# Kernel tuning notes

Hardware: AMD Instinct MI355X
Metric: run time of the kernel (lower is better)

Reference implementation:

```python
import jax, jax.numpy as jnp
import numpy as np

DIM_BODY = 10
DIM_OBJECT = 15
NB_OBJECTS = 3
FIRST_INDS = np.array([0,1,2,3,4,5,6,7,8,9,10,11,12,13,15,16,17,20,21,25])
SECOND_INDS = np.array([0,1,2,3,4,5,6,7,8,9,14,18,19,22,23,24,26,27,28,29])
LOG_SIG_MIN, LOG_SIG_MAX = -20.0, 2.0


def setup_inputs() -> dict:
    key = jax.random.key(0)
    ks = jax.random.split(key, 16)
    B = 65536
    s = 0.05  # weight scale, keeps activations sane
    return {
        "obs": jax.random.normal(ks[0], (B, DIM_BODY + NB_OBJECTS * DIM_OBJECT), jnp.float32),
        "ag": jax.random.normal(ks[1], (B, 30), jnp.float32),
        "g": jax.random.normal(ks[2], (B, 30), jnp.float32),
        "phi_w1": jax.random.normal(ks[3], (80, 256), jnp.float32) * s,
        "phi_b1": jnp.zeros((256,), jnp.float32),
        "phi_w2": jax.random.normal(ks[4], (256, 256), jnp.float32) * s,
        "phi_b2": jnp.zeros((256,), jnp.float32),
        "rho_w1": jax.random.normal(ks[5], (256, 256), jnp.float32) * s,
        "rho_b1": jnp.zeros((256,), jnp.float32),
        "mean_w": jax.random.normal(ks[6], (256, 4), jnp.float32) * s,
        "mean_b": jnp.zeros((4,), jnp.float32),
        "logstd_w": jax.random.normal(ks[7], (256, 4), jnp.float32) * s,
        "logstd_b": jnp.zeros((4,), jnp.float32),
    }


def reference(obs, ag, g, phi_w1, phi_b1, phi_w2, phi_b2, rho_w1, rho_b1,
              mean_w, mean_b, logstd_w, logstd_b):
    body = obs[:, :DIM_BODY]  # [B,10]
    objs = [obs[:, DIM_BODY + DIM_OBJECT * i: DIM_BODY + DIM_OBJECT * (i + 1)]
            for i in range(NB_OBJECTS)]
    ag_f, g_f = ag[:, FIRST_INDS], g[:, FIRST_INDS]
    ag_s, g_s = ag[:, SECOND_INDS], g[:, SECOND_INDS]
    pair_inputs = []
    for i in range(NB_OBJECTS):
        for j in range(NB_OBJECTS):
            if i < j:
                pair_inputs.append(jnp.concatenate([ag_f, body, g_f, objs[i], objs[j]], axis=1))
            elif j < i:
                pair_inputs.append(jnp.concatenate([ag_s, body, g_s, objs[i], objs[j]], axis=1))
    inp = jnp.stack(pair_inputs)  # [6, B, 80]
    # shared phi MLP (2 layers, ReLU on both)
    h = jax.nn.relu(jnp.einsum('pbi,ih->pbh', inp, phi_w1) + phi_b1)
    phi = jax.nn.relu(jnp.einsum('pbh,ho->pbo', h, phi_w2) + phi_b2)
    agg = phi.sum(axis=0)  # [B, 256] sum over pairs
    # rho head
    hr = jax.nn.relu(agg @ rho_w1 + rho_b1)
    mean = hr @ mean_w + mean_b
    logstd = jnp.clip(hr @ logstd_w + logstd_b, LOG_SIG_MIN, LOG_SIG_MAX)
    return mean, logstd
```

## Files before the change

kernel.cpp:

```cpp
#include <hip/hip_runtime.h>
#include <hip/hip_bf16.h>


#define B_TOTAL 65536
#define TROWS   64
#define RSTR    136

typedef __attribute__((ext_vector_type(8))) short s8v;
typedef __attribute__((ext_vector_type(4))) float f4v;

__constant__ int c_PI[6] = {0,0,1,1,2,2};
__constant__ int c_PJ[6] = {1,2,0,2,0,1};
__constant__ int c_PF[6] = {0,0,1,0,1,1};
__constant__ int c_INV[2][30] = {
  {0,1,2,3,4,5,6,7,8,9,10,11,12,13,-1,14,15,16,-1,-1,17,18,-1,-1,-1,19,-1,-1,-1,-1},
  {0,1,2,3,4,5,6,7,8,9,-1,-1,-1,-1,10,-1,-1,-1,11,12,-1,-1,13,14,15,-1,16,17,18,19}};

__global__ void prep_weights(const float* __restrict__ phi_w1,
                             const float* __restrict__ phi_b1,
                             const float* __restrict__ phi_w2,
                             const float* __restrict__ rho_w1,
                             const float* __restrict__ mean_w,
                             const float* __restrict__ logstd_w,
                             __hip_bfloat16* __restrict__ W1P,
                             __hip_bfloat16* __restrict__ W2f,
                             __hip_bfloat16* __restrict__ W3f,
                             __hip_bfloat16* __restrict__ W4f) {
  const int i0 = blockIdx.x * blockDim.x + threadIdx.x;
  const int stride = gridDim.x * blockDim.x;
  for (int d = i0; d < 6 * 32768; d += stride) {
    int p = d >> 15, r = d & 32767;
    int j = r & 7, lane = (r >> 3) & 63, blk = r >> 9;
    int nb = blk >> 2, ks = blk & 3;
    int n = nb * 16 + (lane & 15), k = ks * 32 + (lane >> 4) * 8 + j;
    int f = c_PF[p], oi = c_PI[p], oj = c_PJ[p];
    float v = 0.0f;
    if (k < 30)       { int t = c_INV[f][k];      if (t >= 0) v = phi_w1[t * 256 + n]; }
    else if (k < 60)  { int t = c_INV[f][k - 30]; if (t >= 0) v = phi_w1[(30 + t) * 256 + n]; }
    else if (k < 70)  { v = phi_w1[(20 + k - 60) * 256 + n]; }
    else if (k < 115) { int q = (k - 70) / 15, t = (k - 70) - q * 15;
                        int c = (q == oi) ? 50 + t : (q == oj) ? 65 + t : -1;
                        if (c >= 0) v = phi_w1[c * 256 + n]; }
    else if (k == 115) v = phi_b1[n];
    W1P[d] = __float2bfloat16(v);
  }
  for (int d = i0; d < 65536; d += stride) {
    int j = d & 7, lane = (d >> 3) & 63, blk = d >> 9;
    int nb = blk >> 3, ks = blk & 7;
    int n = nb * 16 + (lane & 15), k = ks * 32 + (lane >> 4) * 8 + j;
    W2f[d] = __float2bfloat16(phi_w2[k * 256 + n]);
    W3f[d] = __float2bfloat16(rho_w1[k * 256 + n]);
  }
  for (int d = i0; d < 4096; d += stride) {
    int j = d & 7, lane = (d >> 3) & 63, ks = d >> 9;
    int n = lane & 15, k = ks * 32 + (lane >> 4) * 8 + j;
    float v = (n < 4) ? mean_w[k * 4 + n]
            : (n < 8) ? logstd_w[k * 4 + (n - 4)] : 0.0f;
    W4f[d] = __float2bfloat16(v);
  }
}

static __device__ __forceinline__ unsigned pk2(float a, float b) {
  __hip_bfloat162 h = __float22bfloat162_rn(float2{a, b});
  union { __hip_bfloat162 h2; unsigned u; } cv; cv.h2 = h;
  return cv.u;
}

__global__ __launch_bounds__(512, 2)
void actor_main(const float* __restrict__ obs, const float* __restrict__ ag,
                const float* __restrict__ g,
                const __hip_bfloat16* __restrict__ W1P,
                const __hip_bfloat16* __restrict__ W2f,
                const __hip_bfloat16* __restrict__ W3f,
                const __hip_bfloat16* __restrict__ W4f,
                const float* __restrict__ b2, const float* __restrict__ b3,
                const float* __restrict__ meanb,
                const float* __restrict__ logstdb,
                float* __restrict__ out) {
  __shared__ __align__(16) __hip_bfloat16 HsBuf[2][4 * 8 * 512];

  const int tid  = threadIdx.x;
  const int lane = tid & 63;
  const int w    = tid >> 6;
  const int l15  = lane & 15;
  const int quad = lane >> 4;
  const int r0   = blockIdx.x * TROWS;

  float4 b2v[2];
#pragma unroll
  for (int i = 0; i < 2; ++i)
    b2v[i] = *(const float4*)&b2[w * 32 + i * 16 + quad * 4];

  s8v w2f[8][2];
#pragma unroll
  for (int i = 0; i < 2; ++i)
#pragma unroll
    for (int ks = 0; ks < 8; ++ks)
      w2f[ks][i] = *(const s8v*)&W2f[(((w * 2 + i) * 8 + ks) * 512) + lane * 8];

  {
    __hip_bfloat16* rawS = &HsBuf[0][0];
    const int row = tid >> 3;
    const int c0  = (tid & 7) * 16;
    const float* agr = ag  + (size_t)(r0 + row) * 30;
    const float* gr  = g   + (size_t)(r0 + row) * 30;
    const float* obr = obs + (size_t)(r0 + row) * 55;
#pragma unroll
    for (int cc = 0; cc < 16; ++cc) {
      int c = c0 + cc;
      float v;
      if      (c < 30)  v = agr[c];
      else if (c < 60)  v = gr[c - 30];
      else if (c < 115) v = obr[c - 60];
      else if (c == 115) v = 1.0f;
      else              v = 0.0f;
      rawS[row * RSTR + c] = __float2bfloat16(v);
    }
  }
  __syncthreads();

  s8v bxr[4][4];
  {
    const __hip_bfloat16* rawS = &HsBuf[0][0];
#pragma unroll
    for (int ks = 0; ks < 4; ++ks)
#pragma unroll
      for (int rt = 0; rt < 4; ++rt)
        bxr[ks][rt] = *(const s8v*)&rawS[(rt * 16 + l15) * RSTR + ks * 32 + quad * 8];
  }
  __syncthreads();

  f4v agg[2][4];
#pragma unroll
  for (int i = 0; i < 2; ++i)
#pragma unroll
    for (int rt = 0; rt < 4; ++rt) agg[i][rt] = f4v{0.f, 0.f, 0.f, 0.f};

  const int ebase = l15 * 8 + (quad >> 1) * 128 + (quad & 1) * 4;

#pragma unroll 1
  for (int p = 0; p < 6; ++p) {
    __hip_bfloat16* buf = &HsBuf[p & 1][0];
    const __hip_bfloat16* w1base = W1P + p * 32768;

#pragma unroll
    for (int i = 0; i < 2; ++i) {
      s8v w1f[4];
#pragma unroll
      for (int ks = 0; ks < 4; ++ks)
        w1f[ks] = *(const s8v*)&w1base[(((w * 2 + i) * 4 + ks) * 512) + lane * 8];
      f4v h[4];
#pragma unroll
      for (int rt = 0; rt < 4; ++rt) h[rt] = f4v{0.f, 0.f, 0.f, 0.f};
#pragma unroll
      for (int ks = 0; ks < 4; ++ks)
#pragma unroll
        for (int rt = 0; rt < 4; ++rt)
          h[rt] = __builtin_amdgcn_mfma_f32_16x16x32_bf16(w1f[ks], bxr[ks][rt], h[rt], 0, 0, 0);
#pragma unroll
      for (int rt = 0; rt < 4; ++rt) {
        float v0 = fmaxf(h[rt][0], 0.f);
        float v1 = fmaxf(h[rt][1], 0.f);
        float v2 = fmaxf(h[rt][2], 0.f);
        float v3 = fmaxf(h[rt][3], 0.f);
        uint2 U; U.x = pk2(v0, v1); U.y = pk2(v2, v3);
        *reinterpret_cast<uint2*>(&buf[(rt * 8 + w) * 512 + i * 256 + ebase]) = U;
      }
    }
    __syncthreads();

    f4v a2[2][4];
#pragma unroll
    for (int i = 0; i < 2; ++i)
#pragma unroll
      for (int rt = 0; rt < 4; ++rt) a2[i][rt] = f4v{0.f, 0.f, 0.f, 0.f};
#pragma unroll
    for (int ks = 0; ks < 8; ++ks) {
      s8v hf[4];
#pragma unroll
      for (int rt = 0; rt < 4; ++rt)
        hf[rt] = *(const s8v*)&buf[(rt * 8 + ks) * 512 + lane * 8];
#pragma unroll
      for (int i = 0; i < 2; ++i)
#pragma unroll
        for (int rt = 0; rt < 4; ++rt)
          a2[i][rt] = __builtin_amdgcn_mfma_f32_16x16x32_bf16(w2f[ks][i], hf[rt], a2[i][rt], 0, 0, 0);
    }
#pragma unroll
    for (int i = 0; i < 2; ++i)
#pragma unroll
      for (int rt = 0; rt < 4; ++rt) {
        agg[i][rt][0] += fmaxf(a2[i][rt][0] + b2v[i].x, 0.f);
        agg[i][rt][1] += fmaxf(a2[i][rt][1] + b2v[i].y, 0.f);
        agg[i][rt][2] += fmaxf(a2[i][rt][2] + b2v[i].z, 0.f);
        agg[i][rt][3] += fmaxf(a2[i][rt][3] + b2v[i].w, 0.f);
      }
  }

  s8v w3f[8][2];
#pragma unroll
  for (int i = 0; i < 2; ++i)
#pragma unroll
    for (int ks = 0; ks < 8; ++ks)
      w3f[ks][i] = *(const s8v*)&W3f[(((w * 2 + i) * 8 + ks) * 512) + lane * 8];
  float4 b3v[2];
#pragma unroll
  for (int i = 0; i < 2; ++i)
    b3v[i] = *(const float4*)&b3[w * 32 + i * 16 + quad * 4];

  {
    __hip_bfloat16* bufA = &HsBuf[0][0];
#pragma unroll
    for (int i = 0; i < 2; ++i)
#pragma unroll
      for (int rt = 0; rt < 4; ++rt) {
        uint2 U; U.x = pk2(agg[i][rt][0], agg[i][rt][1]);
        U.y = pk2(agg[i][rt][2], agg[i][rt][3]);
        *reinterpret_cast<uint2*>(&bufA[(rt * 8 + w) * 512 + i * 256 + ebase]) = U;
      }
  }
  __syncthreads();

  f4v a3[2][4];
#pragma unroll
  for (int i = 0; i < 2; ++i)
#pragma unroll
    for (int rt = 0; rt < 4; ++rt) a3[i][rt] = f4v{0.f, 0.f, 0.f, 0.f};
  {
    const __hip_bfloat16* bufA = &HsBuf[0][0];
#pragma unroll
    for (int ks = 0; ks < 8; ++ks) {
      s8v hf[4];
#pragma unroll
      for (int rt = 0; rt < 4; ++rt)
        hf[rt] = *(const s8v*)&bufA[(rt * 8 + ks) * 512 + lane * 8];
#pragma unroll
      for (int i = 0; i < 2; ++i)
#pragma unroll
        for (int rt = 0; rt < 4; ++rt)
          a3[i][rt] = __builtin_amdgcn_mfma_f32_16x16x32_bf16(w3f[ks][i], hf[rt], a3[i][rt], 0, 0, 0);
    }
  }
  {
    __hip_bfloat16* bufB = &HsBuf[1][0];
#pragma unroll
    for (int i = 0; i < 2; ++i)
#pragma unroll
      for (int rt = 0; rt < 4; ++rt) {
        float v0 = fmaxf(a3[i][rt][0] + b3v[i].x, 0.f);
        float v1 = fmaxf(a3[i][rt][1] + b3v[i].y, 0.f);
        float v2 = fmaxf(a3[i][rt][2] + b3v[i].z, 0.f);
        float v3 = fmaxf(a3[i][rt][3] + b3v[i].w, 0.f);
        uint2 U; U.x = pk2(v0, v1); U.y = pk2(v2, v3);
        *reinterpret_cast<uint2*>(&bufB[(rt * 8 + w) * 512 + i * 256 + ebase]) = U;
      }
  }
  __syncthreads();

  if (w < 4) {
    const __hip_bfloat16* bufB = &HsBuf[1][0];
    f4v a4 = f4v{0.f, 0.f, 0.f, 0.f};
#pragma unroll
    for (int ks = 0; ks < 8; ++ks) {
      s8v w4 = *(const s8v*)&W4f[ks * 512 + lane * 8];
      s8v hf = *(const s8v*)&bufB[(w * 8 + ks) * 512 + lane * 8];
      a4 = __builtin_amdgcn_mfma_f32_16x16x32_bf16(w4, hf, a4, 0, 0, 0);
    }
    const int row = r0 + w * 16 + l15;
    if (quad == 0) {
      float4 mb = *(const float4*)meanb;
      float4 o;
      o.x = a4[0] + mb.x; o.y = a4[1] + mb.y;
      o.z = a4[2] + mb.z; o.w = a4[3] + mb.w;
      *reinterpret_cast<float4*>(&out[(size_t)row * 4]) = o;
    } else if (quad == 1) {
      float4 lb = *(const float4*)logstdb;
      float4 o;
      o.x = fminf(fmaxf(a4[0] + lb.x, -20.f), 2.f);
      o.y = fminf(fmaxf(a4[1] + lb.y, -20.f), 2.f);
      o.z = fminf(fmaxf(a4[2] + lb.z, -20.f), 2.f);
      o.w = fminf(fmaxf(a4[3] + lb.w, -20.f), 2.f);
      *reinterpret_cast<float4*>(&out[(size_t)B_TOTAL * 4 + (size_t)row * 4]) = o;
    }
  }
}

extern "C" void kernel_launch(void* const* d_in, const int* in_sizes, int n_in,
                              void* d_out, int out_size, void* d_ws, size_t ws_size,
                              hipStream_t stream) {
  const float* obs      = (const float*)d_in[0];
  const float* ag       = (const float*)d_in[1];
  const float* g        = (const float*)d_in[2];
  const float* phi_w1   = (const float*)d_in[3];
  const float* phi_b1   = (const float*)d_in[4];
  const float* phi_w2   = (const float*)d_in[5];
  const float* phi_b2   = (const float*)d_in[6];
  const float* rho_w1   = (const float*)d_in[7];
  const float* rho_b1   = (const float*)d_in[8];
  const float* mean_w   = (const float*)d_in[9];
  const float* mean_b   = (const float*)d_in[10];
  const float* logstd_w = (const float*)d_in[11];
  const float* logstd_b = (const float*)d_in[12];
  float* out = (float*)d_out;

  char* ws = (char*)d_ws;
  __hip_bfloat16* W1P = (__hip_bfloat16*)(ws);
  __hip_bfloat16* W2f = (__hip_bfloat16*)(ws + 393216);
  __hip_bfloat16* W3f = (__hip_bfloat16*)(ws + 393216 + 131072);
  __hip_bfloat16* W4f = (__hip_bfloat16*)(ws + 393216 + 262144);

  prep_weights<<<256, 256, 0, stream>>>(phi_w1, phi_b1, phi_w2, rho_w1,
                                        mean_w, logstd_w, W1P, W2f, W3f, W4f);
  actor_main<<<B_TOTAL / TROWS, 512, 0, stream>>>(
      obs, ag, g, W1P, W2f, W3f, W4f, phi_b2, rho_b1, mean_b, logstd_b, out);
}
```

Before: 195.8 us.

## Prefetch next pair's W1 fragments, keep raw inputs in LDS, vectorize prep

Each pair iteration now loads the next pair's layer-1 weight fragments into registers while the current pair computes, hiding global-load latency. Raw inputs move to a dedicated LDS buffer and are re-read per pair instead of being held as 16 register fragments. The input staging and prep_weights kernel now write 16-byte vectors, with prep using one output fragment per wave. The changes trade extra LDS space and reads, plus the double-buffered weight registers, for fewer stalls; register pressure at 512 threads x 2 blocks may spill or cut occupancy.

```diff
diff --git a/kernel.cpp b/kernel.cpp
--- a/kernel.cpp
+++ b/kernel.cpp
@@ -16,48 +16,77 @@
   {0,1,2,3,4,5,6,7,8,9,10,11,12,13,-1,14,15,16,-1,-1,17,18,-1,-1,-1,19,-1,-1,-1,-1},
   {0,1,2,3,4,5,6,7,8,9,-1,-1,-1,-1,10,-1,-1,-1,11,12,-1,-1,13,14,15,-1,16,17,18,19}};
 
-__global__ void prep_weights(const float* __restrict__ phi_w1,
-                             const float* __restrict__ phi_b1,
-                             const float* __restrict__ phi_w2,
-                             const float* __restrict__ rho_w1,
-                             const float* __restrict__ mean_w,
-                             const float* __restrict__ logstd_w,
-                             __hip_bfloat16* __restrict__ W1P,
-                             __hip_bfloat16* __restrict__ W2f,
-                             __hip_bfloat16* __restrict__ W3f,
-                             __hip_bfloat16* __restrict__ W4f) {
-  const int i0 = blockIdx.x * blockDim.x + threadIdx.x;
-  const int stride = gridDim.x * blockDim.x;
-  for (int d = i0; d < 6 * 32768; d += stride) {
-    int p = d >> 15, r = d & 32767;
-    int j = r & 7, lane = (r >> 3) & 63, blk = r >> 9;
-    int nb = blk >> 2, ks = blk & 3;
-    int n = nb * 16 + (lane & 15), k = ks * 32 + (lane >> 4) * 8 + j;
-    int f = c_PF[p], oi = c_PI[p], oj = c_PJ[p];
-    float v = 0.0f;
-    if (k < 30)       { int t = c_INV[f][k];      if (t >= 0) v = phi_w1[t * 256 + n]; }
-    else if (k < 60)  { int t = c_INV[f][k - 30]; if (t >= 0) v = phi_w1[(30 + t) * 256 + n]; }
-    else if (k < 70)  { v = phi_w1[(20 + k - 60) * 256 + n]; }
-    else if (k < 115) { int q = (k - 70) / 15, t = (k - 70) - q * 15;
-                        int c = (q == oi) ? 50 + t : (q == oj) ? 65 + t : -1;
-                        if (c >= 0) v = phi_w1[c * 256 + n]; }
-    else if (k == 115) v = phi_b1[n];
-    W1P[d] = __float2bfloat16(v);
-  }
-  for (int d = i0; d < 65536; d += stride) {
-    int j = d & 7, lane = (d >> 3) & 63, blk = d >> 9;
-    int nb = blk >> 3, ks = blk & 7;
-    int n = nb * 16 + (lane & 15), k = ks * 32 + (lane >> 4) * 8 + j;
-    W2f[d] = __float2bfloat16(phi_w2[k * 256 + n]);
-    W3f[d] = __float2bfloat16(rho_w1[k * 256 + n]);
-  }
-  for (int d = i0; d < 4096; d += stride) {
-    int j = d & 7, lane = (d >> 3) & 63, ks = d >> 9;
-    int n = lane & 15, k = ks * 32 + (lane >> 4) * 8 + j;
-    float v = (n < 4) ? mean_w[k * 4 + n]
-            : (n < 8) ? logstd_w[k * 4 + (n - 4)] : 0.0f;
-    W4f[d] = __float2bfloat16(v);
-  }
+static __device__ __forceinline__ short bf16s(float v) {
+  __hip_bfloat16 h = __float2bfloat16(v);
+  union { __hip_bfloat16 h; short s; } u; u.h = h; return u.s;
+}
+
+__global__ __launch_bounds__(256)
+void prep_weights(const float* __restrict__ phi_w1,
+                  const float* __restrict__ phi_b1,
+                  const float* __restrict__ phi_w2,
+                  const float* __restrict__ rho_w1,
+                  const float* __restrict__ mean_w,
+                  const float* __restrict__ logstd_w,
+                  __hip_bfloat16* __restrict__ W1P,
+                  __hip_bfloat16* __restrict__ W2f,
+                  __hip_bfloat16* __restrict__ W3f,
+                  __hip_bfloat16* __restrict__ W4f) {
+  const int wid  = (blockIdx.x * blockDim.x + threadIdx.x) >> 6;
+  const int lane = threadIdx.x & 63;
+  const int l15  = lane & 15;
+  const int kq   = (lane >> 4) * 8;
+  if (wid >= 648) return;
+  union { short s[8]; s8v v; } o;
+  __hip_bfloat16* dst;
+  if (wid < 384) {
+    const int p = wid >> 6, rem = wid & 63;
+    const int nb = rem >> 2, ks = rem & 3;
+    const int n = nb * 16 + l15;
+    const int f = c_PF[p], oi = c_PI[p], oj = c_PJ[p];
+#pragma unroll
+    for (int j = 0; j < 8; ++j) {
+      int k = ks * 32 + kq + j;
+      float v = 0.0f;
+      if (k < 30)       { int t = c_INV[f][k];      if (t >= 0) v = phi_w1[t * 256 + n]; }
+      else if (k < 60)  { int t = c_INV[f][k - 30]; if (t >= 0) v = phi_w1[(30 + t) * 256 + n]; }
+      else if (k < 70)  { v = phi_w1[(20 + k - 60) * 256 + n]; }
+      else if (k < 115) { int q = (k - 70) / 15, t = (k - 70) - q * 15;
+                          int c = (q == oi) ? 50 + t : (q == oj) ? 65 + t : -1;
+                          if (c >= 0) v = phi_w1[c * 256 + n]; }
+      else if (k == 115) v = phi_b1[n];
+      o.s[j] = bf16s(v);
+    }
+    dst = W1P + wid * 512 + lane * 8;
+  } else if (wid < 512) {
+    const int r = wid - 384;
+    const int nb = r >> 3, ks = r & 7;
+    const int n = nb * 16 + l15;
+#pragma unroll
+    for (int j = 0; j < 8; ++j)
+      o.s[j] = bf16s(phi_w2[(ks * 32 + kq + j) * 256 + n]);
+    dst = W2f + r * 512 + lane * 8;
+  } else if (wid < 640) {
+    const int r = wid - 512;
+    const int nb = r >> 3, ks = r & 7;
+    const int n = nb * 16 + l15;
+#pragma unroll
+    for (int j = 0; j < 8; ++j)
+      o.s[j] = bf16s(rho_w1[(ks * 32 + kq + j) * 256 + n]);
+    dst = W3f + r * 512 + lane * 8;
+  } else {
+    const int ks = wid - 640;
+    const int n = l15;
+#pragma unroll
+    for (int j = 0; j < 8; ++j) {
+      int k = ks * 32 + kq + j;
+      float v = (n < 4) ? mean_w[k * 4 + n]
+              : (n < 8) ? logstd_w[k * 4 + (n - 4)] : 0.0f;
+      o.s[j] = bf16s(v);
+    }
+    dst = W4f + ks * 512 + lane * 8;
+  }
+  *reinterpret_cast<s8v*>(dst) = o.v;
 }
 
 static __device__ __forceinline__ unsigned pk2(float a, float b) {
@@ -77,6 +106,7 @@
                 const float* __restrict__ meanb,
                 const float* __restrict__ logstdb,
                 float* __restrict__ out) {
+  __shared__ __align__(16) __hip_bfloat16 rawS[TROWS * RSTR];
   __shared__ __align__(16) __hip_bfloat16 HsBuf[2][4 * 8 * 512];
 
   const int tid  = threadIdx.x;
@@ -99,12 +129,12 @@
       w2f[ks][i] = *(const s8v*)&W2f[(((w * 2 + i) * 8 + ks) * 512) + lane * 8];
 
   {
-    __hip_bfloat16* rawS = &HsBuf[0][0];
     const int row = tid >> 3;
     const int c0  = (tid & 7) * 16;
     const float* agr = ag  + (size_t)(r0 + row) * 30;
     const float* gr  = g   + (size_t)(r0 + row) * 30;
     const float* obr = obs + (size_t)(r0 + row) * 55;
+    union { short s[16]; s8v v[2]; } o;
 #pragma unroll
     for (int cc = 0; cc < 16; ++cc) {
       int c = c0 + cc;
@@ -114,59 +144,70 @@
       else if (c < 115) v = obr[c - 60];
       else if (c == 115) v = 1.0f;
       else              v = 0.0f;
-      rawS[row * RSTR + c] = __float2bfloat16(v);
-    }
-  }
+      o.s[cc] = bf16s(v);
+    }
+    *reinterpret_cast<s8v*>(&rawS[row * RSTR + c0])     = o.v[0];
+    *reinterpret_cast<s8v*>(&rawS[row * RSTR + c0 + 8]) = o.v[1];
+  }
+
+  s8v w1c[4][2], w1n[4][2];
+#pragma unroll
+  for (int i = 0; i < 2; ++i)
+#pragma unroll
+    for (int ks = 0; ks < 4; ++ks)
+      w1c[ks][i] = *(const s8v*)&W1P[(((w * 2 + i) * 4 + ks) * 512) + lane * 8];
+
+  f4v agg[2][4];
+#pragma unroll
+  for (int i = 0; i < 2; ++i)
+#pragma unroll
+    for (int rt = 0; rt < 4; ++rt) agg[i][rt] = f4v{0.f, 0.f, 0.f, 0.f};
+
+  const int ebase = l15 * 8 + (quad >> 1) * 128 + (quad & 1) * 4;
+
   __syncthreads();
-
-  s8v bxr[4][4];
-  {
-    const __hip_bfloat16* rawS = &HsBuf[0][0];
-#pragma unroll
-    for (int ks = 0; ks < 4; ++ks)
-#pragma unroll
-      for (int rt = 0; rt < 4; ++rt)
-        bxr[ks][rt] = *(const s8v*)&rawS[(rt * 16 + l15) * RSTR + ks * 32 + quad * 8];
-  }
-  __syncthreads();
-
-  f4v agg[2][4];
-#pragma unroll
-  for (int i = 0; i < 2; ++i)
-#pragma unroll
-    for (int rt = 0; rt < 4; ++rt) agg[i][rt] = f4v{0.f, 0.f, 0.f, 0.f};
-
-  const int ebase = l15 * 8 + (quad >> 1) * 128 + (quad & 1) * 4;
 
 #pragma unroll 1
   for (int p = 0; p < 6; ++p) {
     __hip_bfloat16* buf = &HsBuf[p & 1][0];
-    const __hip_bfloat16* w1base = W1P + p * 32768;
-
-#pragma unroll
-    for (int i = 0; i < 2; ++i) {
-      s8v w1f[4];
-#pragma unroll
-      for (int ks = 0; ks < 4; ++ks)
-        w1f[ks] = *(const s8v*)&w1base[(((w * 2 + i) * 4 + ks) * 512) + lane * 8];
-      f4v h[4];
-#pragma unroll
-      for (int rt = 0; rt < 4; ++rt) h[rt] = f4v{0.f, 0.f, 0.f, 0.f};
-#pragma unroll
-      for (int ks = 0; ks < 4; ++ks)
+
+    if (p < 5) {
+      const __hip_bfloat16* nb = W1P + (p + 1) * 32768;
+#pragma unroll
+      for (int i = 0; i < 2; ++i)
+#pragma unroll
+        for (int ks = 0; ks < 4; ++ks)
+          w1n[ks][i] = *(const s8v*)&nb[(((w * 2 + i) * 4 + ks) * 512) + lane * 8];
+    }
+
+    f4v h[2][4];
+#pragma unroll
+    for (int i = 0; i < 2; ++i)
+#pragma unroll
+      for (int rt = 0; rt < 4; ++rt) h[i][rt] = f4v{0.f, 0.f, 0.f, 0.f};
+#pragma unroll
+    for (int ks = 0; ks < 4; ++ks) {
+      s8v bx[4];
+#pragma unroll
+      for (int rt = 0; rt < 4; ++rt)
+        bx[rt] = *(const s8v*)&rawS[(rt * 16 + l15) * RSTR + ks * 32 + quad * 8];
+#pragma unroll
+      for (int i = 0; i < 2; ++i)
 #pragma unroll
         for (int rt = 0; rt < 4; ++rt)
-          h[rt] = __builtin_amdgcn_mfma_f32_16x16x32_bf16(w1f[ks], bxr[ks][rt], h[rt], 0, 0, 0);
+          h[i][rt] = __builtin_amdgcn_mfma_f32_16x16x32_bf16(w1c[ks][i], bx[rt], h[i][rt], 0, 0, 0);
+    }
+#pragma unroll
+    for (int i = 0; i < 2; ++i)
 #pragma unroll
       for (int rt = 0; rt < 4; ++rt) {
-        float v0 = fmaxf(h[rt][0], 0.f);
-        float v1 = fmaxf(h[rt][1], 0.f);
-        float v2 = fmaxf(h[rt][2], 0.f);
-        float v3 = fmaxf(h[rt][3], 0.f);
+        float v0 = fmaxf(h[i][rt][0], 0.f);
+        float v1 = fmaxf(h[i][rt][1], 0.f);
+        float v2 = fmaxf(h[i][rt][2], 0.f);
+        float v3 = fmaxf(h[i][rt][3], 0.f);
         uint2 U; U.x = pk2(v0, v1); U.y = pk2(v2, v3);
         *reinterpret_cast<uint2*>(&buf[(rt * 8 + w) * 512 + i * 256 + ebase]) = U;
       }
-    }
     __syncthreads();
 
     f4v a2[2][4];
@@ -195,6 +236,14 @@
         agg[i][rt][2] += fmaxf(a2[i][rt][2] + b2v[i].z, 0.f);
         agg[i][rt][3] += fmaxf(a2[i][rt][3] + b2v[i].w, 0.f);
       }
+
+    if (p < 5) {
+#pragma unroll
+      for (int i = 0; i < 2; ++i)
+#pragma unroll
+        for (int ks = 0; ks < 4; ++ks)
+          w1c[ks][i] = w1n[ks][i];
+    }
   }
 
   s8v w3f[8][2];
@@ -309,7 +358,7 @@
   __hip_bfloat16* W3f = (__hip_bfloat16*)(ws + 393216 + 131072);
   __hip_bfloat16* W4f = (__hip_bfloat16*)(ws + 393216 + 262144);
 
-  prep_weights<<<256, 256, 0, stream>>>(phi_w1, phi_b1, phi_w2, rho_w1,
+  prep_weights<<<162, 256, 0, stream>>>(phi_w1, phi_b1, phi_w2, rho_w1,
                                         mean_w, logstd_w, W1P, W2f, W3f, W4f);
   actor_main<<<B_TOTAL / TROWS, 512, 0, stream>>>(
       obs, ag, g, W1P, W2f, W3f, W4f, phi_b2, rho_b1, mean_b, logstd_b, out);
```

After: 188.9 us. 1.04x faster.
